# Kernel tuning notes

Measured on AMD Instinct MI355X. Metric: run time of the kernel, lower is better.

The kernel has to match this reference:

```python
import jax, jax.numpy as jnp
import numpy as np

N = 16      # num_nodes
D = 128     # embedding_dim
H = 8       # num_heads
F = 512     # feedforward_dim
L = 4       # num_layers
IN = 64     # per-node input dim (joint_pos 32 + joint_vel 32)
B = 16384   # batch


def _ln(x, g, b):
    m = x.mean(-1, keepdims=True)
    v = ((x - m) ** 2).mean(-1, keepdims=True)
    return (x - m) * jax.lax.rsqrt(v + 1e-5) * g + b


def setup_inputs() -> dict:
    key = jax.random.key(0)
    ks = jax.random.split(key, 24)
    s = 0.02
    inp = {
        'joint_pos': jax.random.normal(ks[0], (B, 32), jnp.float32),
        'joint_vel': jax.random.normal(ks[1], (B, 32), jnp.float32),
        'adjacency': jax.random.randint(ks[2], (N, N), 0, 2).astype(jnp.int32),
        # per-node embedder (distinct Linear per node, stacked)
        'embed_W': jax.random.normal(ks[3], (N, IN, D), jnp.float32) * s,
        'embed_b': jnp.zeros((N, D), jnp.float32),
        'pos_emb': jax.random.normal(ks[4], (N, D), jnp.float32) * s,
        # per-layer attention params, stacked over layer dim
        'Wq': jax.random.normal(ks[5], (L, D, D), jnp.float32) * s,
        'bq': jnp.zeros((L, D), jnp.float32),
        'Wk': jax.random.normal(ks[6], (L, D, D), jnp.float32) * s,
        'bk': jnp.zeros((L, D), jnp.float32),
        'Wv': jax.random.normal(ks[7], (L, D, D), jnp.float32) * s,
        'bv': jnp.zeros((L, D), jnp.float32),
        'Wo': jax.random.normal(ks[8], (L, D, D), jnp.float32) * s,
        'bo': jnp.zeros((L, D), jnp.float32),
        'ln1_g': jnp.ones((L, D), jnp.float32),
        'ln1_b': jnp.zeros((L, D), jnp.float32),
        'ln2_g': jnp.ones((L, D), jnp.float32),
        'ln2_b': jnp.zeros((L, D), jnp.float32),
        'W1': jax.random.normal(ks[9], (L, D, F), jnp.float32) * s,
        'b1': jnp.zeros((L, F), jnp.float32),
        'W2': jax.random.normal(ks[10], (L, F, D), jnp.float32) * s,
        'b2': jnp.zeros((L, D), jnp.float32),
    }
    return inp


def reference(joint_pos, joint_vel, adjacency, embed_W, embed_b, pos_emb,
              Wq, bq, Wk, bk, Wv, bv, Wo, bo,
              ln1_g, ln1_b, ln2_g, ln2_b, W1, b1, W2, b2):
    # adjacency with forced self-loops -> additive attention mask [N, N]
    adj = adjacency.astype(bool) | jnp.eye(N, dtype=bool)
    mask = jnp.where(adj, 0.0, -jnp.inf).astype(jnp.float32)

    # every node sees the full concatenated obs (list-variant obs_node_dict)
    feats = jnp.concatenate([joint_pos, joint_vel], axis=-1)        # [B, IN]
    # distinct per-node linear embedders, batched as one einsum
    x = jnp.einsum('bi,nio->bno', feats, embed_W) + embed_b + pos_emb  # [B, N, D]

    dh = D // H
    scale = 1.0 / (dh ** 0.5)
    for l in range(L):  # BoT-Hard: mask on every layer; pre-LN
        h = _ln(x, ln1_g[l], ln1_b[l])
        q = (h @ Wq[l] + bq[l]).reshape(-1, N, H, dh)
        k = (h @ Wk[l] + bk[l]).reshape(-1, N, H, dh)
        v = (h @ Wv[l] + bv[l]).reshape(-1, N, H, dh)
        s = jnp.einsum('bnhd,bmhd->bhnm', q, k) * scale + mask       # [B, H, N, N]
        a = jax.nn.softmax(s, axis=-1)
        o = jnp.einsum('bhnm,bmhd->bnhd', a, v).reshape(-1, N, D)
        x = x + o @ Wo[l] + bo[l]
        h2 = _ln(x, ln2_g[l], ln2_b[l])
        x = x + jax.nn.relu(h2 @ W1[l] + b1[l]) @ W2[l] + b2[l]
    return x
```

## Files before the change

### kernel.cpp

```cpp
#include <hip/hip_runtime.h>
#include <stdint.h>

typedef __bf16 bf16;
typedef bf16 bf16x8 __attribute__((ext_vector_type(8)));
typedef bf16 bf16x4 __attribute__((ext_vector_type(4)));
typedef float f32x4 __attribute__((ext_vector_type(4)));
typedef uint32_t u32;
typedef uint8_t u8;

#define B_TOT 16384
#define SWG 8
#define NWGS (B_TOT / SWG)

__device__ __forceinline__ f32x4 mfma32(bf16x8 a, bf16x8 b, f32x4 c) {
  return __builtin_amdgcn_mfma_f32_16x16x32_bf16(a, b, c, 0, 0, 0);
}
__device__ __forceinline__ bf16x8 zero8() {
  bf16x8 v;
#pragma unroll
  for (int j = 0; j < 8; j++) v[j] = (bf16)0.f;
  return v;
}

__device__ __forceinline__ void lds_fence() {
  __builtin_amdgcn_sched_barrier(0);
  asm volatile("s_waitcnt lgkmcnt(0)");
  __builtin_amdgcn_sched_barrier(0);
}

__device__ __forceinline__ void stage16(const u8* __restrict__ src, int rowstride, int colbase,
                                        u8* dst, int tid) {
#pragma unroll
  for (int rr = 0; rr < 2; ++rr) {
    u32 o = (u32)(rr * 512 + tid) * 16u;
    u32 row = o >> 7, cb = o & 0x7Fu;
    const u8* s = src + (size_t)row * (size_t)rowstride + (size_t)colbase
                      + (size_t)(cb ^ ((row & 7u) << 4));
    __builtin_amdgcn_global_load_lds((const __attribute__((address_space(1))) u32*)s,
                                     (__attribute__((address_space(3))) u32*)(dst + o),
                                     16, 0, 0);
  }
}

__device__ __forceinline__ void st_row(u8* base, int row, int col, bf16 v) {
  *(bf16*)(base + (u32)(row * 256) + (u32)((2 * col) ^ ((row & 7) << 4))) = v;
}

__device__ __forceinline__ void loadA_rm(const u8* R, int g, int c, bf16x8 a[2][4]) {
  const u32 sw = (u32)(c & 7) << 4;
#pragma unroll
  for (int mt = 0; mt < 2; ++mt)
#pragma unroll
    for (int ks = 0; ks < 4; ++ks)
      a[mt][ks] = *(const bf16x8*)(R + (u32)((mt * 16 + c) * 256)
                                     + (((u32)(ks * 64 + g * 16)) ^ sw));
}

__device__ __forceinline__ void gemm_half(const u8* Wb, int khalf, const bf16x8 a[2][4],
                                          f32x4 acc[2][4], int nh, int g, int c) {
  const u32 sw = (u32)(c & 7) << 4;
#pragma unroll
  for (int ksl = 0; ksl < 2; ++ksl) {
    int ks = khalf * 2 + ksl;
#pragma unroll
    for (int nt = 0; nt < 4; ++nt) {
      bf16x8 b = *(const bf16x8*)(Wb + (u32)((nh * 64 + nt * 16 + c) * 128)
                                     + (((u32)(ksl * 64 + g * 16)) ^ sw));
      acc[0][nt] = mfma32(a[0][ks], b, acc[0][nt]);
      acc[1][nt] = mfma32(a[1][ks], b, acc[1][nt]);
    }
  }
}

template <bool RELU>
__device__ __forceinline__ void epi_rm(const f32x4 acc[2][4], const float* __restrict__ bias,
                                       u8* Rdst, int nh, int g, int c) {
#pragma unroll
  for (int nt = 0; nt < 4; ++nt) {
    int col = nh * 64 + nt * 16 + c;
    float bb = bias[col];
#pragma unroll
    for (int mt = 0; mt < 2; ++mt)
#pragma unroll
      for (int r = 0; r < 4; ++r) {
        float v = acc[mt][nt][r] + bb;
        if (RELU) v = fmaxf(v, 0.f);
        st_row(Rdst, mt * 16 + 4 * g + r, col, (bf16)v);
      }
  }
}

__device__ __forceinline__ void ln_part(const f32x4 x[2][4], float sS[2][4], float sS2[2][4]) {
#pragma unroll
  for (int mt = 0; mt < 2; ++mt) {
    f32x4 a = {0.f, 0.f, 0.f, 0.f}, b = {0.f, 0.f, 0.f, 0.f};
#pragma unroll
    for (int nt = 0; nt < 4; ++nt) { a += x[mt][nt]; b += x[mt][nt] * x[mt][nt]; }
#pragma unroll
    for (int r = 0; r < 4; ++r) {
      float s = a[r], s2 = b[r];
#pragma unroll
      for (int off = 1; off < 16; off <<= 1) { s += __shfl_xor(s, off); s2 += __shfl_xor(s2, off); }
      sS[mt][r] = s; sS2[mt][r] = s2;
    }
  }
}

__global__ void __launch_bounds__(512, 2)
bot_main(const int* __restrict__ adj,
         const float* __restrict__ embB, const float* __restrict__ posE,
         const float* __restrict__ pbq, const float* __restrict__ pbk,
         const float* __restrict__ pbv, const float* __restrict__ pbo,
         const float* __restrict__ l1g, const float* __restrict__ l1b,
         const float* __restrict__ l2g, const float* __restrict__ l2b,
         const float* __restrict__ pb1, const float* __restrict__ pb2,
         const bf16* __restrict__ feats, const bf16* __restrict__ embWT,
         const bf16* __restrict__ wqT, const bf16* __restrict__ wkT,
         const bf16* __restrict__ wvT, const bf16* __restrict__ woT,
         const bf16* __restrict__ w1T, const bf16* __restrict__ w2T,
         float* __restrict__ out) {
  __shared__ u8 smem[163840];
  const int tid = threadIdx.x;
  const int w = tid >> 6, lane = tid & 63, g = lane >> 4, c = lane & 15;
  const int p = w >> 1, nh = w & 1;
  const int S0 = blockIdx.x * SWG;
  const u32 sw = (u32)(c & 7) << 4;

  u8* pairb = smem + p * 32768;
  u8* Rh = pairb;
  u8* Rq = pairb + 8192;
  u8* Rk = pairb + 16384;
  u8* Rv = pairb + 24576;
  u8* WB0 = smem + 131072;
  u8* WB1 = smem + 147456;
  float* scr = (float*)Rk;

  float maskr[4];
#pragma unroll
  for (int r = 0; r < 4; ++r) {
    int n = 4 * g + r;
    maskr[r] = (adj[n * 16 + c] != 0 || n == c) ? 0.f : -1e9f;
  }

  {
    float* x0 = (float*)smem;
    f32x4 ea[16] = {};
    bf16x8 af[2];
#pragma unroll
    for (int ks = 0; ks < 2; ++ks)
      af[ks] = *(const bf16x8*)(feats + (size_t)(S0 + (c & 7)) * 64 + ks * 32 + g * 8);
#pragma unroll
    for (int nt = 0; nt < 16; ++nt) {
#pragma unroll
      for (int ks = 0; ks < 2; ++ks) {
        bf16x8 bw = *(const bf16x8*)(embWT + (size_t)(w * 256 + nt * 16 + c) * 64 + ks * 32 + g * 8);
        ea[nt] = mfma32(af[ks], bw, ea[nt]);
      }
    }
    if (g < 2) {
#pragma unroll
      for (int nt = 0; nt < 16; ++nt)
#pragma unroll
        for (int r = 0; r < 4; ++r)
          x0[(4 * g + r) * 2048 + w * 256 + nt * 16 + c] = ea[nt][r];
    }
  }
  __syncthreads();

  f32x4 x[2][4];
  {
    const float* x0 = (const float*)smem;
#pragma unroll
    for (int nt = 0; nt < 4; ++nt)
#pragma unroll
      for (int r = 0; r < 4; ++r) {
        int n = 4 * g + r, d = nh * 64 + nt * 16 + c;
        float eb = embB[n * 128 + d] + posE[n * 128 + d];
#pragma unroll
        for (int mt = 0; mt < 2; ++mt)
          x[mt][nt][r] = x0[(2 * p + mt) * 2048 + n * 128 + d] + eb;
      }
  }
  __syncthreads();

  bf16x8 Ah[2][4], Ah2[2][4], Au[2][4];

#pragma unroll 1
  for (int l = 0; l < 4; ++l) {
    const u8* Wq_l = (const u8*)(wqT + (size_t)l * 16384);
    const u8* Wk_l = (const u8*)(wkT + (size_t)l * 16384);
    const u8* Wv_l = (const u8*)(wvT + (size_t)l * 16384);
    const u8* Wo_l = (const u8*)(woT + (size_t)l * 16384);
    const u8* W1_l = (const u8*)(w1T + (size_t)l * 65536);
    const u8* W2_l = (const u8*)(w2T + (size_t)l * 65536);

    float sS[2][4], sS2[2][4], mean[2][4], rstd[2][4];

    ln_part(x, sS, sS2);
    if (c == 0) {
#pragma unroll
      for (int mt = 0; mt < 2; ++mt)
#pragma unroll
        for (int r = 0; r < 4; ++r) {
          int row = mt * 16 + 4 * g + r;
          scr[(row * 2 + nh) * 2 + 0] = sS[mt][r];
          scr[(row * 2 + nh) * 2 + 1] = sS2[mt][r];
        }
    }
    __syncthreads();

    stage16(Wq_l, 256, 0, WB0, tid);
#pragma unroll
    for (int mt = 0; mt < 2; ++mt)
#pragma unroll
      for (int r = 0; r < 4; ++r) {
        int row = mt * 16 + 4 * g + r;
        float s = sS[mt][r] + scr[(row * 2 + (1 - nh)) * 2 + 0];
        float s2 = sS2[mt][r] + scr[(row * 2 + (1 - nh)) * 2 + 1];
        float mu = s * (1.f / 128.f);
        float va = s2 * (1.f / 128.f) - mu * mu;
        mean[mt][r] = mu; rstd[mt][r] = rsqrtf(va + 1e-5f);
      }
#pragma unroll
    for (int nt = 0; nt < 4; ++nt) {
      int col = nh * 64 + nt * 16 + c;
      float gg = l1g[l * 128 + col], bb = l1b[l * 128 + col];
#pragma unroll
      for (int mt = 0; mt < 2; ++mt)
#pragma unroll
        for (int r = 0; r < 4; ++r)
          st_row(Rh, mt * 16 + 4 * g + r, col,
                 (bf16)((x[mt][nt][r] - mean[mt][r]) * rstd[mt][r] * gg + bb));
    }
    __syncthreads();

    f32x4 acc[2][4];
    stage16(Wq_l, 256, 128, WB1, tid);
    loadA_rm(Rh, g, c, Ah);
#pragma unroll
    for (int mt = 0; mt < 2; ++mt)
#pragma unroll
      for (int nt = 0; nt < 4; ++nt) acc[mt][nt] = (f32x4){0.f, 0.f, 0.f, 0.f};
    gemm_half(WB0, 0, Ah, acc, nh, g, c);
    __syncthreads();
    stage16(Wk_l, 256, 0, WB0, tid);
    gemm_half(WB1, 1, Ah, acc, nh, g, c);
    epi_rm<false>(acc, pbq + l * 128, Rq, nh, g, c);
    __syncthreads();
    stage16(Wk_l, 256, 128, WB1, tid);
#pragma unroll
    for (int mt = 0; mt < 2; ++mt)
#pragma unroll
      for (int nt = 0; nt < 4; ++nt) acc[mt][nt] = (f32x4){0.f, 0.f, 0.f, 0.f};
    gemm_half(WB0, 0, Ah, acc, nh, g, c);
    __syncthreads();
    stage16(Wv_l, 256, 0, WB0, tid);
    gemm_half(WB1, 1, Ah, acc, nh, g, c);
    epi_rm<false>(acc, pbk + l * 128, Rk, nh, g, c);
    __syncthreads();
    stage16(Wv_l, 256, 128, WB1, tid);
#pragma unroll
    for (int mt = 0; mt < 2; ++mt)
#pragma unroll
      for (int nt = 0; nt < 4; ++nt) acc[mt][nt] = (f32x4){0.f, 0.f, 0.f, 0.f};
    gemm_half(WB0, 0, Ah, acc, nh, g, c);
    __syncthreads();
    gemm_half(WB1, 1, Ah, acc, nh, g, c);
#pragma unroll
    for (int nt = 0; nt < 4; ++nt) {
      int col = nh * 64 + nt * 16 + c;
      float bb = pbv[l * 128 + col];
#pragma unroll
      for (int mt = 0; mt < 2; ++mt) {
        bf16x4 pk;
#pragma unroll
        for (int r = 0; r < 4; ++r) pk[r] = (bf16)(acc[mt][nt][r] + bb);
        *(bf16x4*)(Rv + mt * 4096 + col * 32 + g * 8) = pk;
      }
    }
    __syncthreads();

    stage16(Wo_l, 256, 0, WB0, tid);
    {
      const f32x4 zz = {0.f, 0.f, 0.f, 0.f};
#pragma unroll 1
      for (int hh = 0; hh < 4; ++hh) {
        const int gh = nh * 4 + hh;
        bf16x8 qf[2], kf[2];
#pragma unroll
        for (int mt = 0; mt < 2; ++mt) {
          if (g < 2) {
            qf[mt] = *(const bf16x8*)(Rq + (u32)((mt * 16 + c) * 256)
                                         + (((u32)(gh * 32 + g * 16)) ^ sw));
            kf[mt] = *(const bf16x8*)(Rk + (u32)((mt * 16 + c) * 256)
                                         + (((u32)(gh * 32 + g * 16)) ^ sw));
          } else { qf[mt] = zero8(); kf[mt] = zero8(); }
        }
        f32x4 sc[2];
        sc[0] = mfma32(qf[0], kf[0], zz);
        sc[1] = mfma32(qf[1], kf[1], zz);
        float pr[2][4], mx[2][4], sm[2][4];
#pragma unroll
        for (int mt = 0; mt < 2; ++mt)
#pragma unroll
          for (int r = 0; r < 4; ++r) { pr[mt][r] = sc[mt][r] * 0.25f + maskr[r]; mx[mt][r] = pr[mt][r]; }
#pragma unroll
        for (int off = 1; off < 16; off <<= 1)
#pragma unroll
          for (int mt = 0; mt < 2; ++mt)
#pragma unroll
            for (int r = 0; r < 4; ++r) mx[mt][r] = fmaxf(mx[mt][r], __shfl_xor(mx[mt][r], off));
#pragma unroll
        for (int mt = 0; mt < 2; ++mt)
#pragma unroll
          for (int r = 0; r < 4; ++r) { pr[mt][r] = __expf(pr[mt][r] - mx[mt][r]); sm[mt][r] = pr[mt][r]; }
#pragma unroll
        for (int off = 1; off < 16; off <<= 1)
#pragma unroll
          for (int mt = 0; mt < 2; ++mt)
#pragma unroll
            for (int r = 0; r < 4; ++r) sm[mt][r] += __shfl_xor(sm[mt][r], off);
#pragma unroll
        for (int mt = 0; mt < 2; ++mt)
#pragma unroll
          for (int r = 0; r < 4; ++r)
            st_row(Rq, mt * 16 + 4 * g + r, gh * 16 + c,
                   (bf16)(pr[mt][r] * __fdividef(1.f, sm[mt][r])));
        lds_fence();
        bf16x8 pa[2], vf[2];
#pragma unroll
        for (int mt = 0; mt < 2; ++mt) {
          if (g < 2) {
            pa[mt] = *(const bf16x8*)(Rq + (u32)((mt * 16 + c) * 256)
                                         + (((u32)(gh * 32 + g * 16)) ^ sw));
            vf[mt] = *(const bf16x8*)(Rv + mt * 4096 + gh * 512 + c * 32 + g * 16);
          } else { pa[mt] = zero8(); vf[mt] = zero8(); }
        }
        f32x4 oo[2];
        oo[0] = mfma32(pa[0], vf[0], zz);
        oo[1] = mfma32(pa[1], vf[1], zz);
#pragma unroll
        for (int mt = 0; mt < 2; ++mt)
#pragma unroll
          for (int r = 0; r < 4; ++r)
            st_row(Rq, mt * 16 + 4 * g + r, gh * 16 + c, (bf16)oo[mt][r]);
      }
    }
    __syncthreads();

    stage16(Wo_l, 256, 128, WB1, tid);
    loadA_rm(Rq, g, c, Ah);
    gemm_half(WB0, 0, Ah, x, nh, g, c);
    __syncthreads();
    gemm_half(WB1, 1, Ah, x, nh, g, c);
#pragma unroll
    for (int nt = 0; nt < 4; ++nt) {
      float bb = pbo[l * 128 + nh * 64 + nt * 16 + c];
#pragma unroll
      for (int mt = 0; mt < 2; ++mt)
#pragma unroll
        for (int r = 0; r < 4; ++r) x[mt][nt][r] += bb;
    }
    ln_part(x, sS, sS2);
    if (c == 0) {
#pragma unroll
      for (int mt = 0; mt < 2; ++mt)
#pragma unroll
        for (int r = 0; r < 4; ++r) {
          int row = mt * 16 + 4 * g + r;
          scr[(row * 2 + nh) * 2 + 0] = sS[mt][r];
          scr[(row * 2 + nh) * 2 + 1] = sS2[mt][r];
        }
    }
    __syncthreads();

    stage16(W1_l, 256, 0, WB0, tid);
#pragma unroll
    for (int mt = 0; mt < 2; ++mt)
#pragma unroll
      for (int r = 0; r < 4; ++r) {
        int row = mt * 16 + 4 * g + r;
        float s = sS[mt][r] + scr[(row * 2 + (1 - nh)) * 2 + 0];
        float s2 = sS2[mt][r] + scr[(row * 2 + (1 - nh)) * 2 + 1];
        float mu = s * (1.f / 128.f);
        float va = s2 * (1.f / 128.f) - mu * mu;
        mean[mt][r] = mu; rstd[mt][r] = rsqrtf(va + 1e-5f);
      }
#pragma unroll
    for (int nt = 0; nt < 4; ++nt) {
      int col = nh * 64 + nt * 16 + c;
      float gg = l2g[l * 128 + col], bb = l2b[l * 128 + col];
#pragma unroll
      for (int mt = 0; mt < 2; ++mt)
#pragma unroll
        for (int r = 0; r < 4; ++r)
          st_row(Rh, mt * 16 + 4 * g + r, col,
                 (bf16)((x[mt][nt][r] - mean[mt][r]) * rstd[mt][r] * gg + bb));
    }
    __syncthreads();

#pragma unroll 1
    for (int fc = 0; fc < 4; ++fc) {
      f32x4 uacc[2][4];
#pragma unroll
      for (int mt = 0; mt < 2; ++mt)
#pragma unroll
        for (int nt = 0; nt < 4; ++nt) uacc[mt][nt] = (f32x4){0.f, 0.f, 0.f, 0.f};
      stage16(W1_l + fc * 32768, 256, 128, WB1, tid);
      if (fc == 0) loadA_rm(Rh, g, c, Ah2);
      gemm_half(WB0, 0, Ah2, uacc, nh, g, c);
      __syncthreads();
      stage16(W2_l, 1024, fc * 256, WB0, tid);
      gemm_half(WB1, 1, Ah2, uacc, nh, g, c);
      epi_rm<true>(uacc, pb1 + l * 512 + fc * 128, Rq, nh, g, c);
      __syncthreads();
      stage16(W2_l, 1024, fc * 256 + 128, WB1, tid);
      loadA_rm(Rq, g, c, Au);
      gemm_half(WB0, 0, Au, x, nh, g, c);
      __syncthreads();
      if (fc < 3) stage16(W1_l + (fc + 1) * 32768, 256, 0, WB0, tid);
      gemm_half(WB1, 1, Au, x, nh, g, c);
      __syncthreads();
    }
#pragma unroll
    for (int nt = 0; nt < 4; ++nt) {
      float bb = pb2[l * 128 + nh * 64 + nt * 16 + c];
#pragma unroll
      for (int mt = 0; mt < 2; ++mt)
#pragma unroll
        for (int r = 0; r < 4; ++r) x[mt][nt][r] += bb;
    }
  }

#pragma unroll
  for (int nt = 0; nt < 4; ++nt) {
    int col = nh * 64 + nt * 16 + c;
#pragma unroll
    for (int mt = 0; mt < 2; ++mt)
      *(f32x4*)(pairb + mt * 8192 + col * 64 + g * 16) = x[mt][nt];
  }
  __syncthreads();
  {
    const int smp = S0 + 2 * p + nh;
    const u8* src = pairb + nh * 8192;
#pragma unroll
    for (int it = 0; it < 8; ++it) {
      int n = it * 2 + (lane >> 5);
      int slot = lane & 31;
      f32x4 v;
#pragma unroll
      for (int e = 0; e < 4; ++e)
        v[e] = *(const float*)(src + (u32)((slot * 4 + e) * 64 + n * 4));
      *(f32x4*)(out + (size_t)smp * 2048 + n * 128 + slot * 4) = v;
    }
  }
}

__global__ void prep_feats_k(const float* __restrict__ pos, const float* __restrict__ vel,
                             bf16* __restrict__ feats) {
  int i = blockIdx.x * 256 + threadIdx.x;
  if (i >= B_TOT * 64) return;
  int b = i >> 6, k = i & 63;
  float v = (k < 32) ? pos[b * 32 + k] : vel[b * 32 + (k - 32)];
  feats[i] = (bf16)v;
}

__global__ void prep_tr_k(const float* __restrict__ src, bf16* __restrict__ dst,
                          int R, int C, int total) {
  int i = blockIdx.x * 256 + threadIdx.x;
  if (i >= total) return;
  int rc = R * C;
  int m = i / rc, rem = i % rc;
  int cc = rem / R, rr = rem % R;
  dst[i] = (bf16)src[(size_t)m * rc + rr * C + cc];
}

extern "C" void kernel_launch(void* const* d_in, const int* in_sizes, int n_in,
                              void* d_out, int out_size, void* d_ws, size_t ws_size,
                              hipStream_t stream) {
  const float* jp  = (const float*)d_in[0];
  const float* jv  = (const float*)d_in[1];
  const int*   adj = (const int*)d_in[2];
  const float* eW  = (const float*)d_in[3];
  const float* eB  = (const float*)d_in[4];
  const float* pE  = (const float*)d_in[5];
  const float* Wq  = (const float*)d_in[6];  const float* bq = (const float*)d_in[7];
  const float* Wk  = (const float*)d_in[8];  const float* bk = (const float*)d_in[9];
  const float* Wv  = (const float*)d_in[10]; const float* bv = (const float*)d_in[11];
  const float* Wo  = (const float*)d_in[12]; const float* bo = (const float*)d_in[13];
  const float* g1  = (const float*)d_in[14]; const float* be1 = (const float*)d_in[15];
  const float* g2  = (const float*)d_in[16]; const float* be2 = (const float*)d_in[17];
  const float* W1  = (const float*)d_in[18]; const float* b1 = (const float*)d_in[19];
  const float* W2  = (const float*)d_in[20]; const float* b2 = (const float*)d_in[21];

  bf16* ws    = (bf16*)d_ws;
  bf16* feats = ws;
  bf16* embWT = ws + 1048576;
  bf16* wqT   = embWT + 131072;
  bf16* wkT   = wqT + 65536;
  bf16* wvT   = wkT + 65536;
  bf16* woT   = wvT + 65536;
  bf16* w1T   = woT + 65536;
  bf16* w2T   = w1T + 262144;

  prep_feats_k<<<(B_TOT * 64 + 255) / 256, 256, 0, stream>>>(jp, jv, feats);
  prep_tr_k<<<512, 256, 0, stream>>>(eW, embWT, 64, 128, 131072);
  prep_tr_k<<<256, 256, 0, stream>>>(Wq, wqT, 128, 128, 65536);
  prep_tr_k<<<256, 256, 0, stream>>>(Wk, wkT, 128, 128, 65536);
  prep_tr_k<<<256, 256, 0, stream>>>(Wv, wvT, 128, 128, 65536);
  prep_tr_k<<<256, 256, 0, stream>>>(Wo, woT, 128, 128, 65536);
  prep_tr_k<<<1024, 256, 0, stream>>>(W1, w1T, 128, 512, 262144);
  prep_tr_k<<<1024, 256, 0, stream>>>(W2, w2T, 512, 128, 262144);

  bot_main<<<NWGS, 512, 0, stream>>>(adj, eB, pE, bq, bk, bv, bo,
                                     g1, be1, g2, be2, b1, b2,
                                     feats, embWT, wqT, wkT, wvT, woT, w1T, w2T,
                                     (float*)d_out);
}
```

Baseline: 1.203 ms.

## Quad-buffer weight staging with vmcnt-counted barriers to overlap loads

Grows the weight staging ring from two 16KB buffers to four. Space comes from shrinking each pair's activation region and reusing the LN-output buffer to hold V. Each weight half-tile is now issued one step ahead, and custom barriers wait only with vmcnt(2), so the next tile's global-to-LDS load stays in flight across the barrier instead of draining at every __syncthreads. The risk is subtle LDS reuse hazards and tighter reliance on asm waitcnt ordering, since correctness depends on the exact counting of outstanding loads.

```diff
diff --git a/kernel.cpp b/kernel.cpp
--- a/kernel.cpp
+++ b/kernel.cpp
@@ -24,12 +24,32 @@
 
 __device__ __forceinline__ void lds_fence() {
   __builtin_amdgcn_sched_barrier(0);
-  asm volatile("s_waitcnt lgkmcnt(0)");
+  asm volatile("s_waitcnt lgkmcnt(0)" ::: "memory");
+  __builtin_amdgcn_sched_barrier(0);
+}
+
+__device__ __forceinline__ void bar_lg() {
+  __builtin_amdgcn_sched_barrier(0);
+  asm volatile("s_waitcnt lgkmcnt(0)" ::: "memory");
+  __builtin_amdgcn_s_barrier();
+  __builtin_amdgcn_sched_barrier(0);
+}
+__device__ __forceinline__ void bar_v0() {
+  __builtin_amdgcn_sched_barrier(0);
+  asm volatile("s_waitcnt vmcnt(0) lgkmcnt(0)" ::: "memory");
+  __builtin_amdgcn_s_barrier();
+  __builtin_amdgcn_sched_barrier(0);
+}
+__device__ __forceinline__ void bar_v2() {
+  __builtin_amdgcn_sched_barrier(0);
+  asm volatile("s_waitcnt vmcnt(2) lgkmcnt(0)" ::: "memory");
+  __builtin_amdgcn_s_barrier();
   __builtin_amdgcn_sched_barrier(0);
 }
 
 __device__ __forceinline__ void stage16(const u8* __restrict__ src, int rowstride, int colbase,
                                         u8* dst, int tid) {
+  __builtin_amdgcn_sched_barrier(0);
 #pragma unroll
   for (int rr = 0; rr < 2; ++rr) {
     u32 o = (u32)(rr * 512 + tid) * 16u;
@@ -126,13 +146,14 @@
   const int S0 = blockIdx.x * SWG;
   const u32 sw = (u32)(c & 7) << 4;
 
-  u8* pairb = smem + p * 32768;
-  u8* Rh = pairb;
+  u8* pairb = smem + p * 24576;
+  u8* RA = pairb;
   u8* Rq = pairb + 8192;
   u8* Rk = pairb + 16384;
-  u8* Rv = pairb + 24576;
-  u8* WB0 = smem + 131072;
-  u8* WB1 = smem + 147456;
+  u8* WB0 = smem + 98304;
+  u8* WB1 = smem + 114688;
+  u8* WB2 = smem + 131072;
+  u8* WB3 = smem + 147456;
   float* scr = (float*)Rk;
 
   float maskr[4];
@@ -207,9 +228,9 @@
           scr[(row * 2 + nh) * 2 + 1] = sS2[mt][r];
         }
     }
-    __syncthreads();
-
     stage16(Wq_l, 256, 0, WB0, tid);
+    bar_lg();
+
 #pragma unroll
     for (int mt = 0; mt < 2; ++mt)
 #pragma unroll
@@ -229,42 +250,47 @@
       for (int mt = 0; mt < 2; ++mt)
 #pragma unroll
         for (int r = 0; r < 4; ++r)
-          st_row(Rh, mt * 16 + 4 * g + r, col,
+          st_row(RA, mt * 16 + 4 * g + r, col,
                  (bf16)((x[mt][nt][r] - mean[mt][r]) * rstd[mt][r] * gg + bb));
     }
-    __syncthreads();
+    stage16(Wq_l, 256, 128, WB1, tid);
+    bar_v2();
 
     f32x4 acc[2][4];
-    stage16(Wq_l, 256, 128, WB1, tid);
-    loadA_rm(Rh, g, c, Ah);
+    loadA_rm(RA, g, c, Ah);
 #pragma unroll
     for (int mt = 0; mt < 2; ++mt)
 #pragma unroll
       for (int nt = 0; nt < 4; ++nt) acc[mt][nt] = (f32x4){0.f, 0.f, 0.f, 0.f};
     gemm_half(WB0, 0, Ah, acc, nh, g, c);
-    __syncthreads();
-    stage16(Wk_l, 256, 0, WB0, tid);
+    stage16(Wk_l, 256, 0, WB2, tid);
+    bar_v2();
+
     gemm_half(WB1, 1, Ah, acc, nh, g, c);
     epi_rm<false>(acc, pbq + l * 128, Rq, nh, g, c);
-    __syncthreads();
-    stage16(Wk_l, 256, 128, WB1, tid);
+    stage16(Wk_l, 256, 128, WB3, tid);
+    bar_v2();
+
+#pragma unroll
+    for (int mt = 0; mt < 2; ++mt)
+#pragma unroll
+      for (int nt = 0; nt < 4; ++nt) acc[mt][nt] = (f32x4){0.f, 0.f, 0.f, 0.f};
+    gemm_half(WB2, 0, Ah, acc, nh, g, c);
+    stage16(Wv_l, 256, 0, WB0, tid);
+    bar_v2();
+
+    gemm_half(WB3, 1, Ah, acc, nh, g, c);
+    epi_rm<false>(acc, pbk + l * 128, Rk, nh, g, c);
+    stage16(Wv_l, 256, 128, WB1, tid);
+    bar_v2();
+
 #pragma unroll
     for (int mt = 0; mt < 2; ++mt)
 #pragma unroll
       for (int nt = 0; nt < 4; ++nt) acc[mt][nt] = (f32x4){0.f, 0.f, 0.f, 0.f};
     gemm_half(WB0, 0, Ah, acc, nh, g, c);
-    __syncthreads();
-    stage16(Wv_l, 256, 0, WB0, tid);
-    gemm_half(WB1, 1, Ah, acc, nh, g, c);
-    epi_rm<false>(acc, pbk + l * 128, Rk, nh, g, c);
-    __syncthreads();
-    stage16(Wv_l, 256, 128, WB1, tid);
-#pragma unroll
-    for (int mt = 0; mt < 2; ++mt)
-#pragma unroll
-      for (int nt = 0; nt < 4; ++nt) acc[mt][nt] = (f32x4){0.f, 0.f, 0.f, 0.f};
-    gemm_half(WB0, 0, Ah, acc, nh, g, c);
-    __syncthreads();
+    bar_v0();
+
     gemm_half(WB1, 1, Ah, acc, nh, g, c);
 #pragma unroll
     for (int nt = 0; nt < 4; ++nt) {
@@ -275,12 +301,12 @@
         bf16x4 pk;
 #pragma unroll
         for (int r = 0; r < 4; ++r) pk[r] = (bf16)(acc[mt][nt][r] + bb);
-        *(bf16x4*)(Rv + mt * 4096 + col * 32 + g * 8) = pk;
-      }
-    }
-    __syncthreads();
-
-    stage16(Wo_l, 256, 0, WB0, tid);
+        *(bf16x4*)(RA + mt * 4096 + col * 32 + g * 8) = pk;
+      }
+    }
+    stage16(Wo_l, 256, 0, WB2, tid);
+    bar_lg();
+
     {
       const f32x4 zz = {0.f, 0.f, 0.f, 0.f};
 #pragma unroll 1
@@ -333,7 +359,7 @@
           if (g < 2) {
             pa[mt] = *(const bf16x8*)(Rq + (u32)((mt * 16 + c) * 256)
                                          + (((u32)(gh * 32 + g * 16)) ^ sw));
-            vf[mt] = *(const bf16x8*)(Rv + mt * 4096 + gh * 512 + c * 32 + g * 16);
+            vf[mt] = *(const bf16x8*)(RA + mt * 4096 + gh * 512 + c * 32 + g * 16);
           } else { pa[mt] = zero8(); vf[mt] = zero8(); }
         }
         f32x4 oo[2];
@@ -346,13 +372,14 @@
             st_row(Rq, mt * 16 + 4 * g + r, gh * 16 + c, (bf16)oo[mt][r]);
       }
     }
-    __syncthreads();
-
-    stage16(Wo_l, 256, 128, WB1, tid);
+    stage16(Wo_l, 256, 128, WB3, tid);
+    bar_v2();
+
     loadA_rm(Rq, g, c, Ah);
-    gemm_half(WB0, 0, Ah, x, nh, g, c);
-    __syncthreads();
-    gemm_half(WB1, 1, Ah, x, nh, g, c);
+    gemm_half(WB2, 0, Ah, x, nh, g, c);
+    bar_v0();
+
+    gemm_half(WB3, 1, Ah, x, nh, g, c);
 #pragma unroll
     for (int nt = 0; nt < 4; ++nt) {
       float bb = pbo[l * 128 + nh * 64 + nt * 16 + c];
@@ -372,9 +399,9 @@
           scr[(row * 2 + nh) * 2 + 1] = sS2[mt][r];
         }
     }
-    __syncthreads();
-
     stage16(W1_l, 256, 0, WB0, tid);
+    bar_lg();
+
 #pragma unroll
     for (int mt = 0; mt < 2; ++mt)
 #pragma unroll
@@ -394,10 +421,11 @@
       for (int mt = 0; mt < 2; ++mt)
 #pragma unroll
         for (int r = 0; r < 4; ++r)
-          st_row(Rh, mt * 16 + 4 * g + r, col,
+          st_row(RA, mt * 16 + 4 * g + r, col,
                  (bf16)((x[mt][nt][r] - mean[mt][r]) * rstd[mt][r] * gg + bb));
     }
-    __syncthreads();
+    stage16(W1_l, 256, 128, WB1, tid);
+    bar_v2();
 
 #pragma unroll 1
     for (int fc = 0; fc < 4; ++fc) {
@@ -406,29 +434,31 @@
       for (int mt = 0; mt < 2; ++mt)
 #pragma unroll
         for (int nt = 0; nt < 4; ++nt) uacc[mt][nt] = (f32x4){0.f, 0.f, 0.f, 0.f};
-      stage16(W1_l + fc * 32768, 256, 128, WB1, tid);
-      if (fc == 0) loadA_rm(Rh, g, c, Ah2);
+      if (fc == 0) loadA_rm(RA, g, c, Ah2);
       gemm_half(WB0, 0, Ah2, uacc, nh, g, c);
-      __syncthreads();
-      stage16(W2_l, 1024, fc * 256, WB0, tid);
+      stage16(W2_l, 1024, fc * 256, WB2, tid);
+      bar_v2();
       gemm_half(WB1, 1, Ah2, uacc, nh, g, c);
       epi_rm<true>(uacc, pb1 + l * 512 + fc * 128, Rq, nh, g, c);
-      __syncthreads();
-      stage16(W2_l, 1024, fc * 256 + 128, WB1, tid);
+      stage16(W2_l, 1024, fc * 256 + 128, WB3, tid);
+      bar_v2();
       loadA_rm(Rq, g, c, Au);
-      gemm_half(WB0, 0, Au, x, nh, g, c);
-      __syncthreads();
-      if (fc < 3) stage16(W1_l + (fc + 1) * 32768, 256, 0, WB0, tid);
-      gemm_half(WB1, 1, Au, x, nh, g, c);
-      __syncthreads();
-    }
-#pragma unroll
-    for (int nt = 0; nt < 4; ++nt) {
-      float bb = pb2[l * 128 + nh * 64 + nt * 16 + c];
-#pragma unroll
-      for (int mt = 0; mt < 2; ++mt)
-#pragma unroll
-        for (int r = 0; r < 4; ++r) x[mt][nt][r] += bb;
+      gemm_half(WB2, 0, Au, x, nh, g, c);
+      if (fc < 3) { stage16(W1_l + (fc + 1) * 32768, 256, 0, WB0, tid); bar_v2(); }
+      else bar_v0();
+      gemm_half(WB3, 1, Au, x, nh, g, c);
+      if (fc < 3) { stage16(W1_l + (fc + 1) * 32768, 256, 128, WB1, tid); bar_v2(); }
+      else {
+#pragma unroll
+        for (int nt = 0; nt < 4; ++nt) {
+          float bb = pb2[l * 128 + nh * 64 + nt * 16 + c];
+#pragma unroll
+          for (int mt = 0; mt < 2; ++mt)
+#pragma unroll
+            for (int r = 0; r < 4; ++r) x[mt][nt][r] += bb;
+        }
+        bar_lg();
+      }
     }
   }
 
@@ -439,7 +469,7 @@
     for (int mt = 0; mt < 2; ++mt)
       *(f32x4*)(pairb + mt * 8192 + col * 64 + g * 16) = x[mt][nt];
   }
-  __syncthreads();
+  bar_lg();
   {
     const int smp = S0 + 2 * p + nh;
     const u8* src = pairb + nh * 8192;
```

Measured after the change: 1.159 ms. 3.7% less time.
